# Optimization experiments

Measured on AMD Instinct MI355X. Metric: run time of the kernel, lower is better.

The kernel has to match this reference:

```python
import jax, jax.numpy as jnp
import numpy as np

D_MODEL = 1024
D_STATE = 16
D_CONV = 4
LN_EPS = 1e-5


def setup_inputs() -> dict:
    key = jax.random.key(0)
    ks = jax.random.split(key, 12)
    B, T, D = 2, 2048, D_MODEL
    DI, DS, K = D_MODEL, D_STATE, D_CONV
    s = lambda k, shape, fan: jax.random.normal(k, shape, dtype=jnp.float32) * (1.0 / np.sqrt(fan))
    return {
        "x": jax.random.normal(ks[0], (B, T, D), dtype=jnp.float32),
        "ln_g": jnp.ones((D,), jnp.float32),
        "ln_b": jnp.zeros((D,), jnp.float32),
        "W_in": s(ks[1], (D, 2 * DI), D),          # x @ W_in -> [B,T,2*DI]
        "conv_w": s(ks[2], (DI, 1, K), K),          # depthwise conv kernel (OIH)
        "conv_b": jnp.zeros((DI,), jnp.float32),
        "dt_w": s(ks[3], (DI, DI), DI),
        "dt_b": jnp.zeros((DI,), jnp.float32),
        "B_w": s(ks[4], (DI, DS), DI),
        "C_w": s(ks[5], (DI, DS), DI),
        "log_A": jnp.log(jnp.linspace(1.0, 16.0, DI)).astype(jnp.float32),
        "D_param": jnp.ones((DI,), jnp.float32),
        "W_out": s(ks[6], (DI, D), DI),
    }


def _layernorm(x, g, b):
    mu = jnp.mean(x, axis=-1, keepdims=True)
    var = jnp.mean(jnp.square(x - mu), axis=-1, keepdims=True)
    return (x - mu) * jax.lax.rsqrt(var + LN_EPS) * g + b


def _causal_depthwise_conv(x, w, b):
    # x: [B,T,DI], w: [DI,1,K] -> causal conv, output [B,T,DI]
    xc = jnp.transpose(x, (0, 2, 1))  # [B,DI,T]
    K = w.shape[-1]
    out = jax.lax.conv_general_dilated(
        xc, w, window_strides=(1,), padding=[(K - 1, 0)],
        dimension_numbers=("NCH", "OIH", "NCH"),
        feature_group_count=x.shape[-1])
    return jnp.transpose(out, (0, 2, 1)) + b


def _ssm_scan(x, dt, Bm, Cm, A):
    # x, dt: [B,T,DI]; Bm, Cm: [B,T,DS]; A: [DI]
    Bsz, T, DI = x.shape
    DS = Bm.shape[-1]
    h0 = jnp.zeros((Bsz, DI, DS), jnp.float32)

    def step(h, inp):
        xt, dtt, bt, ct = inp  # [B,DI],[B,DI],[B,DS],[B,DS]
        decay = jnp.exp(jnp.minimum(dtt * A, 0.0))            # [B,DI]
        h = h * decay[..., None] + (dtt * xt)[..., None] * bt[:, None, :]
        y = jnp.einsum("bds,bs->bd", h, ct)
        return h, y

    xs = (jnp.swapaxes(x, 0, 1), jnp.swapaxes(dt, 0, 1),
          jnp.swapaxes(Bm, 0, 1), jnp.swapaxes(Cm, 0, 1))
    _, ys = jax.lax.scan(step, h0, xs)  # ys: [T,B,DI]
    return jnp.swapaxes(ys, 0, 1)


def reference(x, ln_g, ln_b, W_in, conv_w, conv_b, dt_w, dt_b, B_w, C_w, log_A, D_param, W_out):
    residual = x
    xn = _layernorm(x, ln_g, ln_b)
    xz = xn @ W_in                         # [B,T,2*DI]
    x_ssm, z = jnp.split(xz, 2, axis=-1)
    x_ssm = _causal_depthwise_conv(x_ssm, conv_w, conv_b)
    x_ssm = jax.nn.silu(x_ssm)
    dt = jax.nn.softplus(x_ssm @ dt_w + dt_b)   # [B,T,DI]
    Bm = x_ssm @ B_w                            # [B,T,DS]
    Cm = x_ssm @ C_w                            # [B,T,DS]
    A = -jnp.exp(log_A.astype(jnp.float32))     # [DI]
    y = _ssm_scan(x_ssm, dt, Bm, Cm, A)
    y = y + x_ssm * D_param
    y = y * jax.nn.silu(z)
    y = y @ W_out
    return residual + y
```

## Files before the change

kernel.cpp:

```cpp
#include <hip/hip_runtime.h>
#include <cstddef>

#define TSEQ 2048
#define NB   2
#define DM   1024
#define DST  16
#define ROWS (NB*TSEQ)
#define GCH  32
#define LCH  64
#define NDTBC 1152

typedef float  f32x4  __attribute__((ext_vector_type(4)));
typedef short  bf16x8 __attribute__((ext_vector_type(8)));
typedef unsigned short us4 __attribute__((ext_vector_type(4)));
typedef unsigned short u16;

__device__ __forceinline__ float u2f(unsigned short u) {
  return __uint_as_float(((unsigned)u) << 16);
}
__device__ __forceinline__ unsigned short bf16_rn(float x) {
  unsigned u = __float_as_uint(x);
  u += 0x7fff + ((u >> 16) & 1);
  return (unsigned short)(u >> 16);
}
__device__ __forceinline__ void split1(float x, u16& h, u16& l) {
  h = bf16_rn(x);
  l = bf16_rn(x - u2f(h));
}
__device__ __forceinline__ void split4(const float4& v, us4& h, us4& l) {
  u16 h0, h1, h2, h3, l0, l1, l2, l3;
  split1(v.x, h0, l0); split1(v.y, h1, l1);
  split1(v.z, h2, l2); split1(v.w, h3, l3);
  h = (us4){h0, h1, h2, h3};
  l = (us4){l0, l1, l2, l3};
}
__device__ __forceinline__ float softplus_f(float x) {
  return fmaxf(x, 0.0f) + log1pf(expf(-fabsf(x)));
}
__device__ __forceinline__ float silu_f(float x) {
  return x / (1.0f + expf(-x));
}
__device__ __forceinline__ void async16(const void* g, void* l) {
  __builtin_amdgcn_global_load_lds(
      (const __attribute__((address_space(1))) unsigned int*)g,
      (__attribute__((address_space(3))) unsigned int*)l, 16, 0, 0);
}
__device__ __forceinline__ float block_reduce_sum(float v, float* smem) {
#pragma unroll
  for (int off = 32; off > 0; off >>= 1) v += __shfl_down(v, off);
  int wid = threadIdx.x >> 6, lane = threadIdx.x & 63;
  if (lane == 0) smem[wid] = v;
  __syncthreads();
  float r = (smem[0] + smem[1]) + (smem[2] + smem[3]);
  __syncthreads();
  return r;
}

__global__ __launch_bounds__(256) void wsplit_t(const float* __restrict__ W,
    u16* __restrict__ Th, u16* __restrict__ Tl, int K, int N) {
  __shared__ float t[32][33];
  int k0 = blockIdx.y * 32, n0 = blockIdx.x * 32;
  int r = threadIdx.x >> 3, cq = (threadIdx.x & 7) * 4;
  float4 v = *(const float4*)&W[(size_t)(k0 + r) * N + n0 + cq];
  t[r][cq + 0] = v.x; t[r][cq + 1] = v.y; t[r][cq + 2] = v.z; t[r][cq + 3] = v.w;
  __syncthreads();
  int n = threadIdx.x >> 3, kq = (threadIdx.x & 7) * 4;
  float4 w4;
  w4.x = t[kq + 0][n]; w4.y = t[kq + 1][n]; w4.z = t[kq + 2][n]; w4.w = t[kq + 3][n];
  us4 h, l;
  split4(w4, h, l);
  size_t o = (size_t)(n0 + n) * K + k0 + kq;
  *(us4*)&Th[o] = h;
  *(us4*)&Tl[o] = l;
}

__global__ __launch_bounds__(256) void bc_prep(const float* __restrict__ Bw,
    const float* __restrict__ Cw, u16* __restrict__ Th, u16* __restrict__ Tl) {
  int n = DM + blockIdx.x;
  int k = threadIdx.x * 4;
  float4 v = {0.f, 0.f, 0.f, 0.f};
  if (n < DM + DST) {
    int s = n - DM;
    v.x = Bw[(k + 0) * DST + s]; v.y = Bw[(k + 1) * DST + s];
    v.z = Bw[(k + 2) * DST + s]; v.w = Bw[(k + 3) * DST + s];
  } else if (n < DM + 2 * DST) {
    int s = n - DM - DST;
    v.x = Cw[(k + 0) * DST + s]; v.y = Cw[(k + 1) * DST + s];
    v.z = Cw[(k + 2) * DST + s]; v.w = Cw[(k + 3) * DST + s];
  }
  us4 h, l;
  split4(v, h, l);
  size_t o = (size_t)n * DM + k;
  *(us4*)&Th[o] = h;
  *(us4*)&Tl[o] = l;
}

__global__ __launch_bounds__(256) void ln_kernel(const float* __restrict__ x,
    const float* __restrict__ g, const float* __restrict__ b,
    u16* __restrict__ xh, u16* __restrict__ xl) {
  __shared__ float smem[4];
  int r = blockIdx.x;
  size_t base = (size_t)r * DM + threadIdx.x * 4;
  float4 x4 = *(const float4*)&x[base];
  float s = block_reduce_sum(x4.x + x4.y + x4.z + x4.w, smem);
  float mu = s * (1.0f / DM);
  float d0 = x4.x - mu, d1 = x4.y - mu, d2 = x4.z - mu, d3 = x4.w - mu;
  float v = block_reduce_sum(d0*d0 + d1*d1 + d2*d2 + d3*d3, smem) * (1.0f / DM);
  float inv = rsqrtf(v + 1e-5f);
  float4 g4 = *(const float4*)&g[threadIdx.x * 4];
  float4 b4 = *(const float4*)&b[threadIdx.x * 4];
  float4 o;
  o.x = d0 * inv * g4.x + b4.x;
  o.y = d1 * inv * g4.y + b4.y;
  o.z = d2 * inv * g4.z + b4.z;
  o.w = d3 * inv * g4.w + b4.w;
  us4 h, l;
  split4(o, h, l);
  *(us4*)&xh[base] = h;
  *(us4*)&xl[base] = l;
}

template <int EPI>
__global__ __launch_bounds__(256) void gemm_mfma(
    const u16* __restrict__ Ah, const u16* __restrict__ Al,
    const u16* __restrict__ Bh, const u16* __restrict__ Bl,
    float* __restrict__ C, int M, int N, int Kd,
    const float* __restrict__ bias, const float* __restrict__ resid,
    float* __restrict__ C2, float* __restrict__ C3) {
  __shared__ __align__(16) u16 lds[16384];
  int tid = threadIdx.x, wave = tid >> 6, lane = tid & 63;
  int m0 = blockIdx.y * 128, n0 = blockIdx.x * 128;
  int wm = (wave >> 1) * 64, wn = (wave & 1) * 64;
  const u16* srcs[4];
  srcs[0] = Ah + (size_t)m0 * Kd;
  srcs[1] = Al + (size_t)m0 * Kd;
  srcs[2] = Bh + (size_t)n0 * Kd;
  srcs[3] = Bl + (size_t)n0 * Kd;
  const u16* mysrc = srcs[wave] + (size_t)(lane >> 2) * Kd + (lane & 3) * 8;
  u16* myl = lds + wave * 4096;
  const u16* sAh = lds;
  const u16* sAl = lds + 4096;
  const u16* sBh = lds + 8192;
  const u16* sBl = lds + 12288;
  f32x4 acc[4][4];
#pragma unroll
  for (int i = 0; i < 4; ++i)
#pragma unroll
    for (int j = 0; j < 4; ++j) acc[i][j] = (f32x4){0.f, 0.f, 0.f, 0.f};
  int fr = lane & 15, quad = lane >> 4;

  for (int k0 = 0; k0 < Kd; k0 += 32) {
    const u16* s = mysrc + k0;
#pragma unroll
    for (int i = 0; i < 8; ++i)
      async16(s + (size_t)i * 16 * Kd, myl + i * 512);
    __syncthreads();
    bf16x8 afh[4], afl[4], bfh[4], bfl[4];
#pragma unroll
    for (int t = 0; t < 4; ++t) {
      int ro = (wm + t * 16 + fr) * 32 + quad * 8;
      afh[t] = *(const bf16x8*)&sAh[ro];
      afl[t] = *(const bf16x8*)&sAl[ro];
      int co = (wn + t * 16 + fr) * 32 + quad * 8;
      bfh[t] = *(const bf16x8*)&sBh[co];
      bfl[t] = *(const bf16x8*)&sBl[co];
    }
#pragma unroll
    for (int mt = 0; mt < 4; ++mt)
#pragma unroll
      for (int nt = 0; nt < 4; ++nt) {
        acc[mt][nt] = __builtin_amdgcn_mfma_f32_16x16x32_bf16(afh[mt], bfh[nt], acc[mt][nt], 0, 0, 0);
        acc[mt][nt] = __builtin_amdgcn_mfma_f32_16x16x32_bf16(afh[mt], bfl[nt], acc[mt][nt], 0, 0, 0);
        acc[mt][nt] = __builtin_amdgcn_mfma_f32_16x16x32_bf16(afl[mt], bfh[nt], acc[mt][nt], 0, 0, 0);
      }
    __syncthreads();
  }

#pragma unroll
  for (int mt = 0; mt < 4; ++mt)
#pragma unroll
    for (int nt = 0; nt < 4; ++nt) {
      int col = n0 + wn + nt * 16 + fr;
#pragma unroll
      for (int r = 0; r < 4; ++r) {
        int row = m0 + wm + mt * 16 + quad * 4 + r;
        float v = acc[mt][nt][r];
        if (EPI == 2) {
          v += resid[(size_t)row * N + col];
          C[(size_t)row * N + col] = v;
        } else if (EPI == 3) {
          if (col < DM) C[(size_t)row * DM + col] = v;
          else          C2[(size_t)row * DM + col - DM] = v;
        } else if (EPI == 4) {
          if (col < DM) {
            C[(size_t)row * DM + col] = softplus_f(v + bias[col]);
          } else if (col < DM + DST) {
            C2[(size_t)row * DST + col - DM] = v;
          } else if (col < DM + 2 * DST) {
            C3[(size_t)row * DST + col - DM - DST] = v;
          }
        } else {
          C[(size_t)row * N + col] = v;
        }
      }
    }
}

__global__ __launch_bounds__(256) void conv_silu_kernel(
    const float* __restrict__ xin, const float* __restrict__ w,
    const float* __restrict__ cb, u16* __restrict__ xsh, u16* __restrict__ xsl) {
  int r = blockIdx.x;
  int b = r >> 11, t = r & 2047;
  int d = threadIdx.x * 4;
  float4 w0 = *(const float4*)&w[(d + 0) * 4];
  float4 w1 = *(const float4*)&w[(d + 1) * 4];
  float4 w2 = *(const float4*)&w[(d + 2) * 4];
  float4 w3 = *(const float4*)&w[(d + 3) * 4];
  float4 s = *(const float4*)&cb[d];
#pragma unroll
  for (int k = 0; k < 4; ++k) {
    int ts = t + k - 3;
    if (ts >= 0) {
      float4 xv = *(const float4*)&xin[((size_t)(b * TSEQ + ts)) * DM + d];
      s.x = fmaf(xv.x, (&w0.x)[k], s.x);
      s.y = fmaf(xv.y, (&w1.x)[k], s.y);
      s.z = fmaf(xv.z, (&w2.x)[k], s.z);
      s.w = fmaf(xv.w, (&w3.x)[k], s.w);
    }
  }
  float4 o;
  o.x = silu_f(s.x); o.y = silu_f(s.y); o.z = silu_f(s.z); o.w = silu_f(s.w);
  us4 h, l;
  split4(o, h, l);
  size_t base = (size_t)r * DM + d;
  *(us4*)&xsh[base] = h;
  *(us4*)&xsl[base] = l;
}

__global__ __launch_bounds__(256) void scan_a_kernel(
    const float* __restrict__ dt, const u16* __restrict__ xsh,
    const u16* __restrict__ xsl,
    const float* __restrict__ Bm, const float* __restrict__ Cm,
    const float* __restrict__ logA, float* __restrict__ yloc,
    float* __restrict__ cumP, float* __restrict__ hend) {
  int blk = blockIdx.x;
  int dblk = blk & 3, c = (blk >> 2) & 31, b = blk >> 7;
  int di = dblk * 256 + threadIdx.x;
  __shared__ float sB[LCH][DST];
  __shared__ float sC[LCH][DST];
  {
    int tl = threadIdx.x >> 2, sq = (threadIdx.x & 3) * 4;
    size_t base = ((size_t)(b * TSEQ + c * LCH + tl)) * DST + sq;
    *(float4*)&sB[tl][sq] = *(const float4*)&Bm[base];
    *(float4*)&sC[tl][sq] = *(const float4*)&Cm[base];
  }
  __syncthreads();
  float A_di = -expf(logA[di]);
  float h[DST];
#pragma unroll
  for (int s = 0; s < DST; ++s) h[s] = 0.0f;
  float cp = 1.0f;
  for (int tl = 0; tl < LCH; ++tl) {
    size_t idx = ((size_t)(b * TSEQ + c * LCH + tl)) * DM + di;
    float dtv = dt[idx];
    float xv  = u2f(xsh[idx]) + u2f(xsl[idx]);
    float decay = expf(fminf(dtv * A_di, 0.0f));
    float u = dtv * xv;
    float y = 0.0f;
#pragma unroll
    for (int s4 = 0; s4 < 4; ++s4) {
      float4 b4 = *(const float4*)&sB[tl][s4 * 4];
      float4 c4 = *(const float4*)&sC[tl][s4 * 4];
      h[s4*4+0] = fmaf(h[s4*4+0], decay, u * b4.x); y = fmaf(h[s4*4+0], c4.x, y);
      h[s4*4+1] = fmaf(h[s4*4+1], decay, u * b4.y); y = fmaf(h[s4*4+1], c4.y, y);
      h[s4*4+2] = fmaf(h[s4*4+2], decay, u * b4.z); y = fmaf(h[s4*4+2], c4.z, y);
      h[s4*4+3] = fmaf(h[s4*4+3], decay, u * b4.w); y = fmaf(h[s4*4+3], c4.w, y);
    }
    cp *= decay;
    yloc[idx] = y;
    cumP[idx] = cp;
  }
#pragma unroll
  for (int s = 0; s < DST; ++s)
    hend[(((size_t)(b * GCH + c)) * DST + s) * DM + di] = h[s];
}

__global__ __launch_bounds__(256) void scan_b_kernel(
    const float* __restrict__ cumP, float* __restrict__ hboth) {
  int blk = blockIdx.x;
  int dblk = blk & 3, s = (blk >> 2) & 15, b = blk >> 6;
  int di = dblk * 256 + threadIdx.x;
  float H = 0.0f;
  for (int c = 0; c < GCH; ++c) {
    size_t hidx = (((size_t)(b * GCH + c)) * DST + s) * DM + di;
    float e = hboth[hidx];
    hboth[hidx] = H;
    float P = cumP[((size_t)(b * TSEQ + c * LCH + LCH - 1)) * DM + di];
    H = e + P * H;
  }
}

__global__ __launch_bounds__(256) void scan_c_kernel(
    const float* __restrict__ Cm, const float* __restrict__ Hinit,
    const u16* __restrict__ xsh, const u16* __restrict__ xsl,
    const float* __restrict__ zbuf,
    const float* __restrict__ Dp, const float* __restrict__ cumP,
    const float* __restrict__ yloc, u16* __restrict__ yh, u16* __restrict__ yl) {
  int r = blockIdx.x;
  int b = r >> 11, t = r & 2047, c = t >> 6;
  int di = threadIdx.x * 4;
  size_t idx = (size_t)r * DM + di;
  float4 y4 = *(const float4*)&yloc[idx];
  float4 p4 = *(const float4*)&cumP[idx];
  float4 dot = {0.f, 0.f, 0.f, 0.f};
  size_t hbase = ((size_t)(b * GCH + c)) * DST * DM + di;
#pragma unroll
  for (int s = 0; s < DST; ++s) {
    float cs = Cm[(size_t)r * DST + s];
    float4 h4 = *(const float4*)&Hinit[hbase + (size_t)s * DM];
    dot.x = fmaf(cs, h4.x, dot.x);
    dot.y = fmaf(cs, h4.y, dot.y);
    dot.z = fmaf(cs, h4.z, dot.z);
    dot.w = fmaf(cs, h4.w, dot.w);
  }
  y4.x = fmaf(p4.x, dot.x, y4.x);
  y4.y = fmaf(p4.y, dot.y, y4.y);
  y4.z = fmaf(p4.z, dot.z, y4.z);
  y4.w = fmaf(p4.w, dot.w, y4.w);
  us4 xh4 = *(const us4*)&xsh[idx];
  us4 xl4 = *(const us4*)&xsl[idx];
  float4 D4 = *(const float4*)&Dp[di];
  y4.x = fmaf(u2f(xh4.x) + u2f(xl4.x), D4.x, y4.x);
  y4.y = fmaf(u2f(xh4.y) + u2f(xl4.y), D4.y, y4.y);
  y4.z = fmaf(u2f(xh4.z) + u2f(xl4.z), D4.z, y4.z);
  y4.w = fmaf(u2f(xh4.w) + u2f(xl4.w), D4.w, y4.w);
  float4 z4 = *(const float4*)&zbuf[idx];
  y4.x *= silu_f(z4.x);
  y4.y *= silu_f(z4.y);
  y4.z *= silu_f(z4.z);
  y4.w *= silu_f(z4.w);
  us4 h, l;
  split4(y4, h, l);
  *(us4*)&yh[idx] = h;
  *(us4*)&yl[idx] = l;
}

extern "C" void kernel_launch(void* const* d_in, const int* in_sizes, int n_in,
                              void* d_out, int out_size, void* d_ws, size_t ws_size,
                              hipStream_t stream) {
  const float* x      = (const float*)d_in[0];
  const float* ln_g   = (const float*)d_in[1];
  const float* ln_b   = (const float*)d_in[2];
  const float* W_in   = (const float*)d_in[3];
  const float* conv_w = (const float*)d_in[4];
  const float* conv_b = (const float*)d_in[5];
  const float* dt_w   = (const float*)d_in[6];
  const float* dt_b   = (const float*)d_in[7];
  const float* B_w    = (const float*)d_in[8];
  const float* C_w    = (const float*)d_in[9];
  const float* log_A  = (const float*)d_in[10];
  const float* D_par  = (const float*)d_in[11];
  const float* W_out  = (const float*)d_in[12];
  float* out = (float*)d_out;

  float* ws = (float*)d_ws;
  const size_t NE = (size_t)ROWS * DM;
  float* bufX  = ws;
  float* bufZ  = bufX + NE;
  float* bufP  = bufZ + NE;
  float* bufY  = bufP + NE;
  u16*   actH  = (u16*)(bufY + NE);
  u16*   actL  = actH + NE;
  float* bufDT = (float*)(actH + 2 * NE);
  u16*   yH    = (u16*)bufDT;
  u16*   yL    = yH + NE;
  u16* winTh  = (u16*)bufP;
  u16* winTl  = winTh + (size_t)2 * DM * DM;
  u16* dtbcTh = winTl + (size_t)2 * DM * DM;
  u16* dtbcTl = dtbcTh + (size_t)NDTBC * DM;
  float* bufBm = bufX;
  float* bufCm = bufBm + (size_t)ROWS * DST;
  float* bufHe = bufCm + (size_t)ROWS * DST;
  u16* woutTh  = (u16*)(bufHe + (size_t)NB * GCH * DST * DM);
  u16* woutTl  = woutTh + (size_t)DM * DM;

  wsplit_t<<<dim3(2 * DM / 32, DM / 32), 256, 0, stream>>>(W_in, winTh, winTl, DM, 2 * DM);
  wsplit_t<<<dim3(DM / 32, DM / 32), 256, 0, stream>>>(dt_w, dtbcTh, dtbcTl, DM, DM);
  bc_prep<<<NDTBC - DM, 256, 0, stream>>>(B_w, C_w, dtbcTh, dtbcTl);
  ln_kernel<<<ROWS, 256, 0, stream>>>(x, ln_g, ln_b, actH, actL);
  gemm_mfma<3><<<dim3(2 * DM / 128, ROWS / 128), 256, 0, stream>>>(
      actH, actL, winTh, winTl, bufX, ROWS, 2 * DM, DM, nullptr, nullptr, bufZ, nullptr);
  conv_silu_kernel<<<ROWS, 256, 0, stream>>>(bufX, conv_w, conv_b, actH, actL);
  wsplit_t<<<dim3(DM / 32, DM / 32), 256, 0, stream>>>(W_out, woutTh, woutTl, DM, DM);
  gemm_mfma<4><<<dim3(NDTBC / 128, ROWS / 128), 256, 0, stream>>>(
      actH, actL, dtbcTh, dtbcTl, bufDT, ROWS, NDTBC, DM, dt_b, nullptr, bufBm, bufCm);
  scan_a_kernel<<<NB * GCH * 4, 256, 0, stream>>>(bufDT, actH, actL, bufBm, bufCm,
                                                  log_A, bufY, bufP, bufHe);
  scan_b_kernel<<<NB * DST * 4, 256, 0, stream>>>(bufP, bufHe);
  scan_c_kernel<<<ROWS, 256, 0, stream>>>(bufCm, bufHe, actH, actL, bufZ, D_par,
                                          bufP, bufY, yH, yL);
  gemm_mfma<2><<<dim3(DM / 128, ROWS / 128), 256, 0, stream>>>(
      yH, yL, woutTh, woutTl, out, ROWS, DM, DM, nullptr, x, nullptr, nullptr);
}
```

Measured before the change: 368.0 us.

## Double-buffer GEMM LDS loads and shrink N tile to 64 columns

The split-bf16 MFMA GEMM now uses two LDS buffers, so the async global-to-LDS copy of the next K slice is issued before the current slice is computed. This removes the second barrier and is meant to hide load latency behind MFMA work. The block tile changes from 128x128 to 128x64, which doubles the grid size for the three GEMMs and spreads all threads across the loads. Each wave now holds fewer accumulators, which may raise occupancy. In exchange, the A tile is reused across fewer columns, so global traffic for A goes up, and the kernel uses more LDS per block.

```diff
diff --git a/kernel.cpp b/kernel.cpp
--- a/kernel.cpp
+++ b/kernel.cpp
@@ -120,6 +120,7 @@
   *(us4*)&xl[base] = l;
 }
 
+#define LBUF 12288
 template <int EPI>
 __global__ __launch_bounds__(256) void gemm_mfma(
     const u16* __restrict__ Ah, const u16* __restrict__ Al,
@@ -127,40 +128,60 @@
     float* __restrict__ C, int M, int N, int Kd,
     const float* __restrict__ bias, const float* __restrict__ resid,
     float* __restrict__ C2, float* __restrict__ C3) {
-  __shared__ __align__(16) u16 lds[16384];
+  __shared__ __align__(16) u16 lds[2 * LBUF];
   int tid = threadIdx.x, wave = tid >> 6, lane = tid & 63;
-  int m0 = blockIdx.y * 128, n0 = blockIdx.x * 128;
-  int wm = (wave >> 1) * 64, wn = (wave & 1) * 64;
-  const u16* srcs[4];
-  srcs[0] = Ah + (size_t)m0 * Kd;
-  srcs[1] = Al + (size_t)m0 * Kd;
-  srcs[2] = Bh + (size_t)n0 * Kd;
-  srcs[3] = Bl + (size_t)n0 * Kd;
-  const u16* mysrc = srcs[wave] + (size_t)(lane >> 2) * Kd + (lane & 3) * 8;
-  u16* myl = lds + wave * 4096;
-  const u16* sAh = lds;
-  const u16* sAl = lds + 4096;
-  const u16* sBh = lds + 8192;
-  const u16* sBl = lds + 12288;
-  f32x4 acc[4][4];
+  int m0 = blockIdx.y * 128, n0 = blockIdx.x * 64;
+  int wm = (wave >> 1) * 64, wn = (wave & 1) * 32;
+
+  const u16* gptr[6];
+  int ldst[6];
+#pragma unroll
+  for (int r = 0; r < 6; ++r) {
+    int c = r * 256 + tid;
+    int kq = c & 3;
+    const u16* base;
+    int row;
+    if (c < 512)       { base = Ah + (size_t)m0 * Kd; row = c >> 2; }
+    else if (c < 1024) { base = Al + (size_t)m0 * Kd; row = (c - 512) >> 2; }
+    else if (c < 1280) { base = Bh + (size_t)n0 * Kd; row = (c - 1024) >> 2; }
+    else               { base = Bl + (size_t)n0 * Kd; row = (c - 1280) >> 2; }
+    gptr[r] = base + (size_t)row * Kd + kq * 8;
+    ldst[r] = c * 8;
+  }
+
+  f32x4 acc[4][2];
 #pragma unroll
   for (int i = 0; i < 4; ++i)
 #pragma unroll
-    for (int j = 0; j < 4; ++j) acc[i][j] = (f32x4){0.f, 0.f, 0.f, 0.f};
+    for (int j = 0; j < 2; ++j) acc[i][j] = (f32x4){0.f, 0.f, 0.f, 0.f};
   int fr = lane & 15, quad = lane >> 4;
 
-  for (int k0 = 0; k0 < Kd; k0 += 32) {
-    const u16* s = mysrc + k0;
-#pragma unroll
-    for (int i = 0; i < 8; ++i)
-      async16(s + (size_t)i * 16 * Kd, myl + i * 512);
+#pragma unroll
+  for (int r = 0; r < 6; ++r) async16(gptr[r], lds + ldst[r]);
+
+  int nsteps = Kd / 32;
+  for (int s = 0; s < nsteps; ++s) {
+    int cur = (s & 1) * LBUF;
     __syncthreads();
-    bf16x8 afh[4], afl[4], bfh[4], bfl[4];
+    if (s + 1 < nsteps) {
+      int ko = (s + 1) * 32;
+      int nxt = ((s + 1) & 1) * LBUF;
+#pragma unroll
+      for (int r = 0; r < 6; ++r) async16(gptr[r] + ko, lds + nxt + ldst[r]);
+    }
+    const u16* sAh = lds + cur;
+    const u16* sAl = lds + cur + 4096;
+    const u16* sBh = lds + cur + 8192;
+    const u16* sBl = lds + cur + 10240;
+    bf16x8 afh[4], afl[4], bfh[2], bfl[2];
 #pragma unroll
     for (int t = 0; t < 4; ++t) {
       int ro = (wm + t * 16 + fr) * 32 + quad * 8;
       afh[t] = *(const bf16x8*)&sAh[ro];
       afl[t] = *(const bf16x8*)&sAl[ro];
+    }
+#pragma unroll
+    for (int t = 0; t < 2; ++t) {
       int co = (wn + t * 16 + fr) * 32 + quad * 8;
       bfh[t] = *(const bf16x8*)&sBh[co];
       bfl[t] = *(const bf16x8*)&sBl[co];
@@ -168,18 +189,17 @@
 #pragma unroll
     for (int mt = 0; mt < 4; ++mt)
 #pragma unroll
-      for (int nt = 0; nt < 4; ++nt) {
+      for (int nt = 0; nt < 2; ++nt) {
         acc[mt][nt] = __builtin_amdgcn_mfma_f32_16x16x32_bf16(afh[mt], bfh[nt], acc[mt][nt], 0, 0, 0);
         acc[mt][nt] = __builtin_amdgcn_mfma_f32_16x16x32_bf16(afh[mt], bfl[nt], acc[mt][nt], 0, 0, 0);
         acc[mt][nt] = __builtin_amdgcn_mfma_f32_16x16x32_bf16(afl[mt], bfh[nt], acc[mt][nt], 0, 0, 0);
       }
-    __syncthreads();
   }
 
 #pragma unroll
   for (int mt = 0; mt < 4; ++mt)
 #pragma unroll
-    for (int nt = 0; nt < 4; ++nt) {
+    for (int nt = 0; nt < 2; ++nt) {
       int col = n0 + wn + nt * 16 + fr;
 #pragma unroll
       for (int r = 0; r < 4; ++r) {
@@ -388,17 +408,17 @@
   wsplit_t<<<dim3(DM / 32, DM / 32), 256, 0, stream>>>(dt_w, dtbcTh, dtbcTl, DM, DM);
   bc_prep<<<NDTBC - DM, 256, 0, stream>>>(B_w, C_w, dtbcTh, dtbcTl);
   ln_kernel<<<ROWS, 256, 0, stream>>>(x, ln_g, ln_b, actH, actL);
-  gemm_mfma<3><<<dim3(2 * DM / 128, ROWS / 128), 256, 0, stream>>>(
+  gemm_mfma<3><<<dim3(2 * DM / 64, ROWS / 128), 256, 0, stream>>>(
       actH, actL, winTh, winTl, bufX, ROWS, 2 * DM, DM, nullptr, nullptr, bufZ, nullptr);
   conv_silu_kernel<<<ROWS, 256, 0, stream>>>(bufX, conv_w, conv_b, actH, actL);
   wsplit_t<<<dim3(DM / 32, DM / 32), 256, 0, stream>>>(W_out, woutTh, woutTl, DM, DM);
-  gemm_mfma<4><<<dim3(NDTBC / 128, ROWS / 128), 256, 0, stream>>>(
+  gemm_mfma<4><<<dim3(NDTBC / 64, ROWS / 128), 256, 0, stream>>>(
       actH, actL, dtbcTh, dtbcTl, bufDT, ROWS, NDTBC, DM, dt_b, nullptr, bufBm, bufCm);
   scan_a_kernel<<<NB * GCH * 4, 256, 0, stream>>>(bufDT, actH, actL, bufBm, bufCm,
                                                   log_A, bufY, bufP, bufHe);
   scan_b_kernel<<<NB * DST * 4, 256, 0, stream>>>(bufP, bufHe);
   scan_c_kernel<<<ROWS, 256, 0, stream>>>(bufCm, bufHe, actH, actL, bufZ, D_par,
                                           bufP, bufY, yH, yL);
-  gemm_mfma<2><<<dim3(DM / 128, ROWS / 128), 256, 0, stream>>>(
+  gemm_mfma<2><<<dim3(DM / 64, ROWS / 128), 256, 0, stream>>>(
       yH, yL, woutTh, woutTl, out, ROWS, DM, DM, nullptr, x, nullptr, nullptr);
 }
```

New measurement: 349.6 us. -5.0%, faster.
